# Optimization experiments

Hardware: AMD Instinct MI355X
Metric: run time of the kernel (lower is better)

Reference implementation:

```python
import jax, jax.numpy as jnp
import numpy as np

GROUPS = 2
EPS = 1e-5


def channel_shuffle(x, groups=2):
    b, c, h, w = x.shape
    x = x.reshape(b, groups, c // groups, h, w)
    x = jnp.transpose(x, (0, 2, 1, 3, 4))
    return x.reshape(b, c, h, w)


def binarize_weight(w):
    # w: (O, I/g, k, k). scaling_factor = mean |w| over (in,kh,kw), detached.
    scale = jax.lax.stop_gradient(jnp.mean(jnp.abs(w), axis=(1, 2, 3), keepdims=True))
    bw = scale * jnp.sign(w)
    cl = jnp.clip(w, -1.0, 1.0)
    # STE: forward value = bw, gradient flows through clamp
    return jax.lax.stop_gradient(bw) - jax.lax.stop_gradient(cl) + cl


@jax.custom_vjp
def bin_act(x):
    return jnp.sign(x)


def _bin_act_fwd(x):
    return jnp.sign(x), x


def _bin_act_bwd(x, g):
    scale = jnp.where((x >= 1.0) | (x <= -1.0), 0.01, 1.0)
    return (g * scale,)


bin_act.defvjp(_bin_act_fwd, _bin_act_bwd)


def grouped_bin_conv(x, w, pad):
    return jax.lax.conv_general_dilated(
        x, binarize_weight(w), window_strides=(1, 1),
        padding=[(pad, pad), (pad, pad)],
        dimension_numbers=('NCHW', 'OIHW', 'NCHW'),
        feature_group_count=GROUPS)


def batchnorm(x, gamma, beta):
    # training-mode BN: biased batch statistics over (N,H,W)
    mu = jnp.mean(x, axis=(0, 2, 3), keepdims=True)
    var = jnp.mean((x - mu) ** 2, axis=(0, 2, 3), keepdims=True)
    xn = (x - mu) * jax.lax.rsqrt(var + EPS)
    return xn * gamma[None, :, None, None] + beta[None, :, None, None]


def add_bias(x, b):
    return x + b[None, :, None, None]


def prelu(x, a):
    return jnp.where(x >= 0, x, a[None, :, None, None] * x)


def setup_inputs() -> dict:
    key = jax.random.key(0)
    ks = jax.random.split(key, 4)
    C, half = 256, 128
    x = jax.random.normal(ks[0], (32, C, 56, 56), dtype=jnp.float32)
    # two BinaryConvs (64,128,3,3) stacked -> grouped (128,128,3,3)
    w3 = jax.random.uniform(ks[1], (half, C // GROUPS, 3, 3), dtype=jnp.float32) * 0.001
    w1 = jax.random.uniform(ks[2], (half, C // GROUPS, 1, 1), dtype=jnp.float32) * 0.001
    z = jnp.zeros((C,), jnp.float32)
    return {
        'x': x, 'w3': w3, 'w1': w1,
        'b1': z, 'g1': jnp.ones((half,), jnp.float32), 'be1': jnp.zeros((half,), jnp.float32),
        'b2_1': z, 'a2': jnp.full((C,), 0.25, jnp.float32), 'b2_2': z,
        'b3_1': z, 'g3': jnp.ones((half,), jnp.float32), 'be3': jnp.zeros((half,), jnp.float32),
        'b4_1': z, 'a4': jnp.full((C,), 0.25, jnp.float32), 'b4_2': z,
    }


def reference(x, w3, w1, b1, g1, be1, b2_1, a2, b2_2, b3_1, g3, be3, b4_1, a4, b4_2):
    half = w3.shape[0]  # out_channel // 2 = 128
    x = channel_shuffle(x, GROUPS)
    x1 = bin_act(add_bias(x, b1))
    x1 = batchnorm(grouped_bin_conv(x1, w3, pad=1), g1, be1)
    x1_res = x[:, half:]
    x1 = x1 + x[:, :half]
    x2 = jnp.concatenate([x1, x1_res], axis=1)
    x2 = add_bias(prelu(add_bias(x2, b2_1), a2), b2_2)
    x2 = add_bias(x2, b3_1)
    x3 = bin_act(x2)
    x3 = batchnorm(grouped_bin_conv(x3, w1, pad=0), g3, be3)
    x3_res = x2[:, half:]
    x3 = x3 + x2[:, :half]
    x4 = jnp.concatenate([x3, x3_res], axis=1)
    x5 = add_bias(prelu(add_bias(x4, b4_1), a4), b4_2)
    return x5
```

## Files before the change

kernel.cpp:

```cpp
#include <hip/hip_runtime.h>
#include <stdint.h>

typedef unsigned short ushort_t;
typedef unsigned int uint_t;
typedef _Float16 half_t;

typedef float  float4_t __attribute__((ext_vector_type(4)));
typedef float  float2_t __attribute__((ext_vector_type(2)));
typedef _Float16 half4_t __attribute__((ext_vector_type(4)));
typedef _Float16 half2_t __attribute__((ext_vector_type(2)));
typedef uint_t uint4_t  __attribute__((ext_vector_type(4)));
typedef uint_t uint2_t  __attribute__((ext_vector_type(2)));

#define B_N 32
#define C_N 256
#define HALF_N 128
#define H_N 56
#define W_N 56
#define HW_N 3136
#define NPIX (B_N * HW_N)
#define EPS_D 1e-5
#define W3S 40
#define PWS 16

__global__ void prep_kernel(const float* __restrict__ w3, const float* __restrict__ w1,
                            uint_t* __restrict__ wbits3, uint_t* __restrict__ wbits1,
                            uint_t* __restrict__ popcw3,
                            double* __restrict__ scale3, double* __restrict__ scale1,
                            double* __restrict__ sums1, double* __restrict__ sums2,
                            uint_t* __restrict__ oflags) {
    __shared__ double red[128];
    __shared__ int ipw[2][9];
    __shared__ int flsh[2];
    int t = threadIdx.x;
    int blk = blockIdx.x;
    int lane = t & 63;
    int wv = t >> 6;
    if (blk == 0) {
        sums1[t] = 0.0; sums1[128 + t] = 0.0;
        sums2[t] = 0.0; sums2[128 + t] = 0.0;
    }
    if (blk < 128) {
        int o = blk;
        double acc = 0.0;
        int anynp = 0;
        #pragma unroll
        for (int j = 0; j < 9; ++j) {
            float v = w3[o * 1152 + t * 9 + j];
            acc += fabs((double)v);
            anynp |= (v <= 0.f) ? 1 : 0;
            unsigned long long b = __ballot(v > 0.f);
            if (lane == 0) {
                wbits3[o * W3S + j * 4 + wv * 2 + 0] = (uint_t)b;
                wbits3[o * W3S + j * 4 + wv * 2 + 1] = (uint_t)(b >> 32);
                ipw[wv][j] = __popcll(b);
            }
        }
        unsigned long long m = __ballot(anynp != 0);
        if (lane == 0) flsh[wv] = (m != 0ull) ? 1 : 0;
        red[t] = acc; __syncthreads();
        for (int s = 64; s > 0; s >>= 1) { if (t < s) red[t] += red[t + s]; __syncthreads(); }
        if (t == 0) { scale3[o] = red[0] / 1152.0; oflags[o] = (uint_t)(flsh[0] | flsh[1]); }
        if (t < 9) popcw3[o * PWS + t] = (uint_t)(ipw[0][t] + ipw[1][t]);
    } else {
        int o = blk - 128;
        float v = w1[o * 128 + t];
        unsigned long long b = __ballot(v > 0.f);
        unsigned long long m = __ballot(v <= 0.f);
        if (lane == 0) {
            wbits1[o * 8 + wv * 2 + 0] = (uint_t)b;
            wbits1[o * 8 + wv * 2 + 1] = (uint_t)(b >> 32);
            flsh[wv] = (m != 0ull) ? 1 : 0;
        }
        red[t] = fabs((double)v); __syncthreads();
        for (int s = 64; s > 0; s >>= 1) { if (t < s) red[t] += red[t + s]; __syncthreads(); }
        if (t == 0) { scale1[o] = red[0] / 128.0; oflags[128 + o] = (uint_t)(flsh[0] | flsh[1]); }
    }
}

__global__ __launch_bounds__(256) void sign1_kernel(const float* __restrict__ x,
                                                    const float* __restrict__ b1,
                                                    uint_t* __restrict__ vb,
                                                    const uint_t* __restrict__ oflags,
                                                    uint_t* __restrict__ fin) {
    __shared__ int fl[4];
    int t = threadIdx.x;
    if (blockIdx.x == 0 && blockIdx.y == 0) {
        int lane = t & 63, wv4 = t >> 6;
        uint_t f = oflags[t];
        unsigned long long m = __ballot(f != 0u);
        if (lane == 0) fl[wv4] = (m != 0ull) ? 1 : 0;
        __syncthreads();
        if (t == 0) { fin[0] = (uint_t)(fl[0] | fl[1]); fin[1] = (uint_t)(fl[2] | fl[3]); }
    }
    int p = blockIdx.x * 512 + t * 2;
    int cb = blockIdx.y * 32;
    int b = p / HW_N;
    int hw = p - b * HW_N;
    const float* xb = x + (size_t)b * C_N * HW_N + hw;
    uint_t w0 = 0, w1 = 0;
    #pragma unroll
    for (int j = 0; j < 32; ++j) {
        int c = cb + j;
        int src = ((c & 1) << 7) + (c >> 1);
        float2_t xv = *(const float2_t*)(xb + (size_t)src * HW_N);
        double bc = (double)b1[c];
        if ((double)xv[0] + bc > 0.0) w0 |= (1u << j);
        if ((double)xv[1] + bc > 0.0) w1 |= (1u << j);
    }
    uint2_t o2; o2[0] = w0; o2[1] = w1;
    *(uint2_t*)(vb + (size_t)(cb >> 5) * NPIX + p) = o2;
}

__global__ __launch_bounds__(256) void conv3_kernel(const uint_t* __restrict__ vb,
                                                    const uint_t* __restrict__ wbits3,
                                                    const uint_t* __restrict__ popcw3,
                                                    half_t* __restrict__ yh,
                                                    double* __restrict__ sums,
                                                    const uint_t* __restrict__ fin) {
    __shared__ short dlds[32][258];
    __shared__ int partS[8][32];
    __shared__ int partS2[8][32];
    int t = threadIdx.x;
    int lane = t & 63;
    int wv = t >> 6;
    bool fast = (fin[0] == 0u);
    int yb = blockIdx.y;
    if (fast && (yb & 1)) return;
    int g = yb >> 1;
    int oh = yb & 1;
    int o0 = g * 64 + oh * 32;
    int p = blockIdx.x * 256 + t;
    int hw = p % HW_N;
    int h = hw / W_N;
    int w = hw - h * W_N;
    const uint_t* vbase = vb + (size_t)g * 4 * NPIX;

    uint_t v[9][4];
    int inv[9];
    int nvalid = 0;
    #pragma unroll
    for (int j = 0; j < 9; ++j) {
        int kh = j / 3 - 1, kw = j - (j / 3) * 3 - 1;
        int hh = h + kh, ww = w + kw;
        bool valid = (hh >= 0) && (hh < H_N) && (ww >= 0) && (ww < W_N);
        inv[j] = valid ? 0 : 1;
        nvalid += valid ? 1 : 0;
        int off = p + kh * W_N + kw;
        #pragma unroll
        for (int q = 0; q < 4; ++q)
            v[j][q] = valid ? vbase[(size_t)q * NPIX + off] : 0u;
    }
    int base = 128 * nvalid;

    if (fast) {
        int P = 0;
        #pragma unroll
        for (int j = 0; j < 9; ++j)
            #pragma unroll
            for (int q = 0; q < 4; ++q)
                P += __popc(v[j][q]);
        int dot = 2 * P - base;
        yh[(size_t)o0 * NPIX + p] = (half_t)(float)dot;
        int s = dot, s2 = dot * dot;
        #pragma unroll
        for (int off = 32; off > 0; off >>= 1) {
            s  += __shfl_xor(s, off);
            s2 += __shfl_xor(s2, off);
        }
        if (lane == 0) { partS[0][wv] = s; partS2[0][wv] = s2; }
        __syncthreads();
        if (t == 0) {
            partS[1][0]  = partS[0][0] + partS[0][1] + partS[0][2] + partS[0][3];
            partS2[1][0] = partS2[0][0] + partS2[0][1] + partS2[0][2] + partS2[0][3];
        }
        __syncthreads();
        if (t < 64) {
            atomicAdd(&sums[o0 + t], (double)partS[1][0]);
            atomicAdd(&sums[128 + o0 + t], (double)partS2[1][0]);
        }
        return;
    }

    half_t* yrow = yh + (size_t)o0 * NPIX + p;
    for (int oi = 0; oi < 32; ++oi) {
        const uint_t* wo = wbits3 + (size_t)(o0 + oi) * W3S;
        const uint_t* pw = popcw3 + (size_t)(o0 + oi) * PWS;
        int acc = 0;
        #pragma unroll
        for (int j = 0; j < 9; ++j)
            #pragma unroll
            for (int q = 0; q < 4; ++q)
                acc += __popc(v[j][q] ^ wo[j * 4 + q]);
        int corr = 0;
        #pragma unroll
        for (int j = 0; j < 9; ++j) corr += inv[j] * (int)pw[j];
        int dot = base - 2 * (acc - corr);
        yrow[(size_t)oi * NPIX] = (half_t)(float)dot;
        dlds[oi][t] = (short)dot;
    }
    __syncthreads();
    {
        int o = t & 31, seg = t >> 5;
        const int* r32 = (const int*)(&dlds[o][seg * 32]);
        int S = 0, S2 = 0;
        #pragma unroll
        for (int j = 0; j < 16; ++j) {
            int pr = r32[j];
            int d0 = (int)(short)(pr & 0xffff);
            int d1 = pr >> 16;
            S += d0 + d1; S2 += d0 * d0 + d1 * d1;
        }
        partS[seg][o] = S; partS2[seg][o] = S2;
    }
    __syncthreads();
    if (t < 32) {
        int S = 0, S2 = 0;
        #pragma unroll
        for (int s8 = 0; s8 < 8; ++s8) { S += partS[s8][t]; S2 += partS2[s8][t]; }
        int c = o0 + t;
        atomicAdd(&sums[c], (double)S);
        atomicAdd(&sums[128 + c], (double)S2);
    }
}

__device__ __forceinline__ void coef_entry(const double* __restrict__ sums,
                                           const double* __restrict__ scale,
                                           const float* __restrict__ gamma,
                                           const float* __restrict__ beta,
                                           int c, double* coefL) {
    double M = (double)NPIX;
    double mean = sums[c] / M;
    double var = sums[128 + c] / M - mean * mean;
    double s = scale[c];
    double r = 1.0 / sqrt(s * s * var + EPS_D);
    double g = (double)gamma[c];
    coefL[c] = s * r * g;
    coefL[128 + c] = (double)beta[c] - s * mean * r * g;
}

__device__ __forceinline__ void coef_entry_f(const double* __restrict__ sums,
                                             const double* __restrict__ scale,
                                             const float* __restrict__ gamma,
                                             const float* __restrict__ beta,
                                             int c, float* cf) {
    double M = (double)NPIX;
    double mean = sums[c] / M;
    double var = sums[128 + c] / M - mean * mean;
    double s = scale[c];
    double r = 1.0 / sqrt(s * s * var + EPS_D);
    double g = (double)gamma[c];
    cf[c] = (float)(s * r * g);
    cf[128 + c] = (float)((double)beta[c] - s * mean * r * g);
}

__device__ __forceinline__ double x2_val(double xs, double K, bool hasy,
                                         const double* coef1, int c,
                                         const float* __restrict__ b2_1, const float* __restrict__ a2,
                                         const float* __restrict__ b2_2, const float* __restrict__ b3_1) {
    int ci = c & 127;
    double t = hasy ? (coef1[ci] * K + coef1[128 + ci] + xs) : xs;
    t += (double)b2_1[c];
    double a = (double)a2[c];
    t = (t >= 0.0) ? t : a * t;
    t += (double)b2_2[c];
    t += (double)b3_1[c];
    return t;
}

__global__ __launch_bounds__(256, 4) void x2c1_fast_kernel(
        const float* __restrict__ x, const half_t* __restrict__ y1h,
        const double* __restrict__ sums1, const double* __restrict__ scale3,
        const float* __restrict__ g1, const float* __restrict__ be1,
        const float* __restrict__ b2_1, const float* __restrict__ a2,
        const float* __restrict__ b2_2, const float* __restrict__ b3_1,
        half_t* __restrict__ y3h, double* __restrict__ sums2,
        const float* __restrict__ b4_1, const float* __restrict__ a4,
        const float* __restrict__ b4_2, float* __restrict__ out,
        const uint_t* __restrict__ fin) {
    if ((fin[0] | fin[1]) != 0u) return;
    __shared__ float tile[64][128];
    __shared__ double coefL[256];
    __shared__ uint_t shW[128][5];
    __shared__ int red[4];
    int t = threadIdx.x;
    int lane = t & 63;
    int w = t >> 6;
    int g = blockIdx.y;
    if (g == 0 && t < 128) coef_entry(sums1, scale3, g1, be1, t, coefL);

    int p0 = blockIdx.x * 128;
    int sp = p0 + 2 * lane;
    int sb = sp / HW_N;
    int shw = sp - sb * HW_N;
    const float* sbase = x + (size_t)sb * C_N * HW_N + shw;
    int pl = t & 127;
    int h = t >> 7;
    int p = p0 + pl;
    int b = p / HW_N;
    int hw = p - b * HW_N;
    __syncthreads();

    uint_t wd0 = 0, wd1 = 0;
    #pragma unroll
    for (int cp = 0; cp < 2; ++cp) {
        #pragma unroll
        for (int s = 0; s < 16; ++s) {
            int cl = w + 4 * s;
            int c = g * 128 + cp * 64 + cl;
            int src = ((c & 1) << 7) + (c >> 1);
            float2_t v = *(const float2_t*)(sbase + (size_t)src * HW_N);
            *(float2_t*)(&tile[cl][2 * lane]) = v;
        }
        __syncthreads();
        double K = 0.0;
        if (g == 0) K = (double)(float)y1h[(size_t)(cp * 64) * NPIX + p];
        uint_t bits = 0u;
        #pragma unroll
        for (int j = 0; j < 32; ++j) {
            int cl = h * 32 + j;
            int c = g * 128 + cp * 64 + cl;
            double xs = (double)tile[cl][pl];
            double v = x2_val(xs, K, g == 0, coefL, c, b2_1, a2, b2_2, b3_1);
            bits |= (v > 0.0) ? (1u << j) : 0u;
            if (g == 1) {
                float b41c = b4_1[c], a4c = a4[c], b42c = b4_2[c];
                float f0 = (float)v + b41c;
                f0 = (f0 >= 0.f) ? f0 : a4c * f0;
                f0 += b42c;
                out[((size_t)b * C_N + c) * HW_N + hw] = f0;
            }
        }
        shW[pl][cp * 2 + h] = bits;
        if (cp == 0) wd0 = bits; else wd1 = bits;
        (void)wd0; (void)wd1;
        __syncthreads();
    }

    uint_t W0 = shW[pl][0], W1 = shW[pl][1], W2 = shW[pl][2], W3 = shW[pl][3];
    int P = __popc(W0) + __popc(W1) + __popc(W2) + __popc(W3);
    int dot = 2 * P - 128;
    int obase = g * 64;
    if (h == 0) y3h[(size_t)obase * NPIX + p] = (half_t)(float)dot;
    int s = dot, s2 = dot * dot;
    #pragma unroll
    for (int off = 32; off > 0; off >>= 1) {
        s  += __shfl_xor(s, off);
        s2 += __shfl_xor(s2, off);
    }
    if (h == 0 && lane == 0) { red[w] = s; red[2 + w] = s2; }
    __syncthreads();
    if (t < 64) {
        int S  = red[0] + red[1];
        int S2 = red[2] + red[3];
        atomicAdd(&sums2[obase + t], (double)S);
        atomicAdd(&sums2[128 + obase + t], (double)S2);
    }
}

__global__ __launch_bounds__(256) void x2c1_gen_kernel(
        const float* __restrict__ x, const half_t* __restrict__ y1h,
        const double* __restrict__ sums1, const double* __restrict__ scale3,
        const float* __restrict__ g1, const float* __restrict__ be1,
        const float* __restrict__ b2_1, const float* __restrict__ a2,
        const float* __restrict__ b2_2, const float* __restrict__ b3_1,
        const uint_t* __restrict__ wbits1,
        half_t* __restrict__ y3h, double* __restrict__ sums2,
        const float* __restrict__ b4_1, const float* __restrict__ a4,
        const float* __restrict__ b4_2, float* __restrict__ out,
        const uint_t* __restrict__ fin) {
    if ((fin[0] | fin[1]) == 0u) return;
    __shared__ double coefL[256];
    __shared__ uint_t shW[128][5];
    __shared__ short dst[64][130];
    __shared__ int partS[4][64];
    __shared__ int partS2[4][64];
    int t = threadIdx.x;
    int lane = t & 63;
    int wv = t >> 6;
    int pl = t & 127;
    int ch = t >> 7;
    int g = blockIdx.y;
    bool fast3 = (fin[0] == 0u);
    bool fast1 = (fin[1] == 0u);
    if (g == 0 && t < 128) coef_entry(sums1, scale3, g1, be1, t, coefL);
    __syncthreads();

    int p = blockIdx.x * 128 + pl;
    int b = p / HW_N;
    int hw = p - b * HW_N;
    const float* xb = x + (size_t)b * C_N * HW_N + hw;

    uint_t wA = 0, wB = 0;
    if (g == 0) {
        if (fast3) {
            double K = (double)(float)y1h[(size_t)(ch * 64) * NPIX + p];
            #pragma unroll
            for (int wq = 0; wq < 2; ++wq) {
                uint_t bits = 0u;
                #pragma unroll
                for (int j = 0; j < 32; ++j) {
                    int c = ch * 64 + wq * 32 + j;
                    int src = ((c & 1) << 7) + (c >> 1);
                    double xs = (double)xb[(size_t)src * HW_N];
                    double v = x2_val(xs, K, true, coefL, c, b2_1, a2, b2_2, b3_1);
                    bits |= (v > 0.0) ? (1u << j) : 0u;
                }
                if (wq == 0) wA = bits; else wB = bits;
            }
        } else {
            #pragma unroll
            for (int wq = 0; wq < 2; ++wq) {
                uint_t bits = 0u;
                #pragma unroll
                for (int j = 0; j < 32; ++j) {
                    int c = ch * 64 + wq * 32 + j;
                    int src = ((c & 1) << 7) + (c >> 1);
                    double xs = (double)xb[(size_t)src * HW_N];
                    double K = (double)(float)y1h[(size_t)c * NPIX + p];
                    double v = x2_val(xs, K, true, coefL, c, b2_1, a2, b2_2, b3_1);
                    bits |= (v > 0.0) ? (1u << j) : 0u;
                }
                if (wq == 0) wA = bits; else wB = bits;
            }
        }
    } else {
        #pragma unroll
        for (int wq = 0; wq < 2; ++wq) {
            uint_t bits = 0u;
            #pragma unroll
            for (int j = 0; j < 32; ++j) {
                int c = 128 + ch * 64 + wq * 32 + j;
                int src = ((c & 1) << 7) + (c >> 1);
                double xs = (double)xb[(size_t)src * HW_N];
                double v = x2_val(xs, 0.0, false, coefL, c, b2_1, a2, b2_2, b3_1);
                bits |= (v > 0.0) ? (1u << j) : 0u;
                float b41c = b4_1[c], a4c = a4[c], b42c = b4_2[c];
                float f0 = (float)v + b41c;
                f0 = (f0 >= 0.f) ? f0 : a4c * f0;
                f0 += b42c;
                out[((size_t)b * C_N + c) * HW_N + hw] = f0;
            }
            if (wq == 0) wA = bits; else wB = bits;
        }
    }

    shW[pl][2 * ch + 0] = wA;
    shW[pl][2 * ch + 1] = wB;
    __syncthreads();
    uint_t W0 = shW[pl][0], W1 = shW[pl][1], W2 = shW[pl][2], W3 = shW[pl][3];

    int obase = g * 64;
    if (fast1) {
        if (ch == 0) {
            int P = __popc(W0) + __popc(W1) + __popc(W2) + __popc(W3);
            int dot = 2 * P - 128;
            y3h[(size_t)obase * NPIX + p] = (half_t)(float)dot;
            int s = dot, s2 = dot * dot;
            #pragma unroll
            for (int off = 32; off > 0; off >>= 1) {
                s  += __shfl_xor(s, off);
                s2 += __shfl_xor(s2, off);
            }
            if (lane == 0) { partS[0][wv] = s; partS2[0][wv] = s2; }
        }
        __syncthreads();
        if (t == 0) {
            partS[1][0]  = partS[0][0] + partS[0][1];
            partS2[1][0] = partS2[0][0] + partS2[0][1];
        }
        __syncthreads();
        if (t < 64) {
            atomicAdd(&sums2[obase + t], (double)partS[1][0]);
            atomicAdd(&sums2[128 + obase + t], (double)partS2[1][0]);
        }
        return;
    }

    #pragma unroll
    for (int oi = 0; oi < 32; ++oi) {
        int o = obase + ch * 32 + oi;
        const uint_t* wo = wbits1 + (size_t)o * 8;
        int acc = __popc(W0 ^ wo[0]) + __popc(W1 ^ wo[1])
                + __popc(W2 ^ wo[2]) + __popc(W3 ^ wo[3]);
        int dot = 128 - 2 * acc;
        y3h[(size_t)o * NPIX + p] = (half_t)(float)dot;
        dst[ch * 32 + oi][pl] = (short)dot;
    }
    __syncthreads();
    {
        int o = t & 63, seg = t >> 6;
        const int* r32 = (const int*)(&dst[o][seg * 32]);
        int S = 0, S2 = 0;
        #pragma unroll
        for (int j = 0; j < 16; ++j) {
            int pr = r32[j];
            int e0 = (int)(short)(pr & 0xffff);
            int e1 = pr >> 16;
            S += e0 + e1; S2 += e0 * e0 + e1 * e1;
        }
        partS[seg][o] = S; partS2[seg][o] = S2;
    }
    __syncthreads();
    if (t < 64) {
        int S  = partS[0][t] + partS[1][t] + partS[2][t] + partS[3][t];
        int S2 = partS2[0][t] + partS2[1][t] + partS2[2][t] + partS2[3][t];
        int c = obase + t;
        atomicAdd(&sums2[c], (double)S);
        atomicAdd(&sums2[128 + c], (double)S2);
    }
}

__global__ __launch_bounds__(256) void out_kernel(
        const float* __restrict__ x, const half_t* __restrict__ y1h,
        const half_t* __restrict__ y3h,
        const double* __restrict__ sums1, const double* __restrict__ scale3,
        const float* __restrict__ g1, const float* __restrict__ be1,
        const double* __restrict__ sums2, const double* __restrict__ scale1,
        const float* __restrict__ g3, const float* __restrict__ be3,
        const float* __restrict__ b2_1, const float* __restrict__ a2,
        const float* __restrict__ b2_2, const float* __restrict__ b3_1,
        const float* __restrict__ b4_1, const float* __restrict__ a4,
        const float* __restrict__ b4_2, float* __restrict__ out,
        const uint_t* __restrict__ fin) {
    __shared__ float c1f[256];
    __shared__ float c3f[256];
    int t = threadIdx.x;
    if (t < 128) coef_entry_f(sums1, scale3, g1, be1, t, c1f);
    else coef_entry_f(sums2, scale1, g3, be3, t - 128, c3f);
    __syncthreads();
    int c = blockIdx.y;
    int src = ((c & 1) << 7) + (c >> 1);
    int y1slice = (fin[0] == 0u) ? ((c < 64) ? 0 : 64) : c;
    int y3slice = (fin[1] == 0u) ? ((c < 64) ? 0 : 64) : c;
    float b21 = b2_1[c], aa2v = a2[c], b23 = b2_2[c] + b3_1[c];
    float b41 = b4_1[c], aa4v = a4[c], b42 = b4_2[c];
    float c1 = c1f[c], c1b = c1f[128 + c];
    float c3 = c3f[c], c3b = c3f[128 + c];
    const half_t* y1p = y1h + (size_t)y1slice * NPIX;
    const half_t* y3p = y3h + (size_t)y3slice * NPIX;
    #pragma unroll
    for (int i = 0; i < 2; ++i) {
        int p = blockIdx.x * 2048 + i * 1024 + t * 4;
        int b = p / HW_N;
        int hw = p - b * HW_N;
        float4_t xs = *(const float4_t*)(x + ((size_t)b * C_N + src) * HW_N + hw);
        half4_t y1v = *(const half4_t*)(y1p + p);
        half4_t y3v = *(const half4_t*)(y3p + p);
        float4_t ov;
        #pragma unroll
        for (int k = 0; k < 4; ++k) {
            float v = fmaf(c1, (float)y1v[k], c1b) + xs[k];
            v += b21;
            v = (v >= 0.f) ? v : aa2v * v;
            v += b23;
            float t2 = v;
            v = fmaf(c3, (float)y3v[k], c3b) + t2;
            v += b41;
            v = (v >= 0.f) ? v : aa4v * v;
            v += b42;
            ov[k] = v;
        }
        *(float4_t*)(out + ((size_t)b * C_N + c) * HW_N + hw) = ov;
    }
}

extern "C" void kernel_launch(void* const* d_in, const int* in_sizes, int n_in,
                              void* d_out, int out_size, void* d_ws, size_t ws_size,
                              hipStream_t stream) {
    const float* x    = (const float*)d_in[0];
    const float* w3   = (const float*)d_in[1];
    const float* w1   = (const float*)d_in[2];
    const float* b1   = (const float*)d_in[3];
    const float* g1   = (const float*)d_in[4];
    const float* be1  = (const float*)d_in[5];
    const float* b2_1 = (const float*)d_in[6];
    const float* a2   = (const float*)d_in[7];
    const float* b2_2 = (const float*)d_in[8];
    const float* b3_1 = (const float*)d_in[9];
    const float* g3   = (const float*)d_in[10];
    const float* be3  = (const float*)d_in[11];
    const float* b4_1 = (const float*)d_in[12];
    const float* a4   = (const float*)d_in[13];
    const float* b4_2 = (const float*)d_in[14];

    char* ws = (char*)d_ws;
    half_t* y1h    = (half_t*)(ws + 0);
    half_t* y3h    = (half_t*)(ws + 25690112);
    uint_t* wbits3 = (uint_t*)(ws + 51380224);
    uint_t* wbits1 = (uint_t*)(ws + 51400704);
    uint_t* popcw3 = (uint_t*)(ws + 51404800);
    double* scale3 = (double*)(ws + 51412992);
    double* scale1 = (double*)(ws + 51414016);
    double* sums1  = (double*)(ws + 51415040);
    double* sums2  = (double*)(ws + 51417088);
    uint_t* oflags = (uint_t*)(ws + 51419136);
    uint_t* fin    = (uint_t*)(ws + 51420160);

    uint_t* vb1 = (uint_t*)((char*)d_out + 0);
    float*  outp = (float*)d_out;

    prep_kernel<<<256, 128, 0, stream>>>(w3, w1, wbits3, wbits1, popcw3,
                                         scale3, scale1, sums1, sums2, oflags);
    sign1_kernel<<<dim3(NPIX / 512, 8), 256, 0, stream>>>(x, b1, vb1, oflags, fin);
    conv3_kernel<<<dim3(NPIX / 256, 4), 256, 0, stream>>>(vb1, wbits3, popcw3, y1h, sums1, fin);
    x2c1_fast_kernel<<<dim3(NPIX / 128, 2), 256, 0, stream>>>(x, y1h, sums1, scale3, g1, be1,
                                                              b2_1, a2, b2_2, b3_1,
                                                              y3h, sums2,
                                                              b4_1, a4, b4_2, outp, fin);
    x2c1_gen_kernel<<<dim3(NPIX / 128, 2), 256, 0, stream>>>(x, y1h, sums1, scale3, g1, be1,
                                                             b2_1, a2, b2_2, b3_1,
                                                             wbits1, y3h, sums2,
                                                             b4_1, a4, b4_2, outp, fin);
    out_kernel<<<dim3(NPIX / 2048, 128), 256, 0, stream>>>(x, y1h, y3h,
                                                           sums1, scale3, g1, be1,
                                                           sums2, scale1, g3, be3,
                                                           b2_1, a2, b2_2, b3_1,
                                                           b4_1, a4, b4_2, outp, fin);
}
```

Measured before the change: 316.4 us.

## Split fused x2/conv1 fast kernel into per-group kernels without LDS transpose tile

Replaces the single two-group fast kernel with two separate kernels, one per channel group. Each handles 64 pixels per block with four channel quarters, reading x directly instead of staging it through a shared-memory tile. This drops the 32KB LDS tile, the branch on group inside the hot loop and the cross-wave reduction, and lifts the forced occupancy hint. The cost is an extra launch, narrower per-thread global reads, and twice as many sums2 atomics, since each block covers 64 pixels instead of 128.

Measured after the change: 336.7 us. +6.4%, slower.

```diff
diff --git a/kernel.cpp b/kernel.cpp
--- a/kernel.cpp
+++ b/kernel.cpp
@@ -268,10 +268,56 @@
     return t;
 }
 
-__global__ __launch_bounds__(256, 4) void x2c1_fast_kernel(
+__global__ __launch_bounds__(256) void x2g0_fast_kernel(
         const float* __restrict__ x, const half_t* __restrict__ y1h,
         const double* __restrict__ sums1, const double* __restrict__ scale3,
         const float* __restrict__ g1, const float* __restrict__ be1,
+        const float* __restrict__ b2_1, const float* __restrict__ a2,
+        const float* __restrict__ b2_2, const float* __restrict__ b3_1,
+        half_t* __restrict__ y3h, double* __restrict__ sums2,
+        const uint_t* __restrict__ fin) {
+    if ((fin[0] | fin[1]) != 0u) return;
+    __shared__ double coefL[256];
+    __shared__ uint_t shW[64][5];
+    int t = threadIdx.x;
+    if (t < 128) coef_entry(sums1, scale3, g1, be1, t, coefL);
+    __syncthreads();
+    int ql = t & 63;
+    int qc = t >> 6;
+    int p = blockIdx.x * 64 + ql;
+    int b = p / HW_N;
+    int hw = p - b * HW_N;
+    const float* xb = x + (size_t)b * C_N * HW_N + hw;
+    double K = (double)(float)y1h[(size_t)((qc >> 1) * 64) * NPIX + p];
+    uint_t bits = 0u;
+    #pragma unroll
+    for (int j = 0; j < 32; ++j) {
+        int c = qc * 32 + j;
+        int src = ((c & 1) << 7) + (c >> 1);
+        double xs = (double)xb[(size_t)src * HW_N];
+        double v = x2_val(xs, K, true, coefL, c, b2_1, a2, b2_2, b3_1);
+        bits |= (v > 0.0) ? (1u << j) : 0u;
+    }
+    shW[ql][qc] = bits;
+    __syncthreads();
+    if (t < 64) {
+        uint_t W0 = shW[t][0], W1 = shW[t][1], W2 = shW[t][2], W3 = shW[t][3];
+        int P = __popc(W0) + __popc(W1) + __popc(W2) + __popc(W3);
+        int dot = 2 * P - 128;
+        y3h[p] = (half_t)(float)dot;
+        int s = dot, s2 = dot * dot;
+        #pragma unroll
+        for (int off = 32; off > 0; off >>= 1) {
+            s  += __shfl_xor(s, off);
+            s2 += __shfl_xor(s2, off);
+        }
+        atomicAdd(&sums2[t], (double)s);
+        atomicAdd(&sums2[128 + t], (double)s2);
+    }
+}
+
+__global__ __launch_bounds__(256) void x2g1_fast_kernel(
+        const float* __restrict__ x,
         const float* __restrict__ b2_1, const float* __restrict__ a2,
         const float* __restrict__ b2_2, const float* __restrict__ b3_1,
         half_t* __restrict__ y3h, double* __restrict__ sums2,
@@ -279,82 +325,47 @@
         const float* __restrict__ b4_2, float* __restrict__ out,
         const uint_t* __restrict__ fin) {
     if ((fin[0] | fin[1]) != 0u) return;
-    __shared__ float tile[64][128];
-    __shared__ double coefL[256];
-    __shared__ uint_t shW[128][5];
-    __shared__ int red[4];
+    __shared__ uint_t shW[64][5];
     int t = threadIdx.x;
-    int lane = t & 63;
-    int w = t >> 6;
-    int g = blockIdx.y;
-    if (g == 0 && t < 128) coef_entry(sums1, scale3, g1, be1, t, coefL);
-
-    int p0 = blockIdx.x * 128;
-    int sp = p0 + 2 * lane;
-    int sb = sp / HW_N;
-    int shw = sp - sb * HW_N;
-    const float* sbase = x + (size_t)sb * C_N * HW_N + shw;
-    int pl = t & 127;
-    int h = t >> 7;
-    int p = p0 + pl;
+    int ql = t & 63;
+    int qc = t >> 6;
+    int p = blockIdx.x * 64 + ql;
     int b = p / HW_N;
     int hw = p - b * HW_N;
-    __syncthreads();
-
-    uint_t wd0 = 0, wd1 = 0;
+    const float* xb = x + (size_t)b * C_N * HW_N + hw;
+    uint_t bits = 0u;
     #pragma unroll
-    for (int cp = 0; cp < 2; ++cp) {
-        #pragma unroll
-        for (int s = 0; s < 16; ++s) {
-            int cl = w + 4 * s;
-            int c = g * 128 + cp * 64 + cl;
-            int src = ((c & 1) << 7) + (c >> 1);
-            float2_t v = *(const float2_t*)(sbase + (size_t)src * HW_N);
-            *(float2_t*)(&tile[cl][2 * lane]) = v;
-        }
-        __syncthreads();
-        double K = 0.0;
-        if (g == 0) K = (double)(float)y1h[(size_t)(cp * 64) * NPIX + p];
-        uint_t bits = 0u;
-        #pragma unroll
-        for (int j = 0; j < 32; ++j) {
-            int cl = h * 32 + j;
-            int c = g * 128 + cp * 64 + cl;
-            double xs = (double)tile[cl][pl];
-            double v = x2_val(xs, K, g == 0, coefL, c, b2_1, a2, b2_2, b3_1);
-            bits |= (v > 0.0) ? (1u << j) : 0u;
-            if (g == 1) {
-                float b41c = b4_1[c], a4c = a4[c], b42c = b4_2[c];
-                float f0 = (float)v + b41c;
-                f0 = (f0 >= 0.f) ? f0 : a4c * f0;
-                f0 += b42c;
-                out[((size_t)b * C_N + c) * HW_N + hw] = f0;
-            }
-        }
-        shW[pl][cp * 2 + h] = bits;
-        if (cp == 0) wd0 = bits; else wd1 = bits;
-        (void)wd0; (void)wd1;
-        __syncthreads();
-    }
-
-    uint_t W0 = shW[pl][0], W1 = shW[pl][1], W2 = shW[pl][2], W3 = shW[pl][3];
-    int P = __popc(W0) + __popc(W1) + __popc(W2) + __popc(W3);
-    int dot = 2 * P - 128;
-    int obase = g * 64;
-    if (h == 0) y3h[(size_t)obase * NPIX + p] = (half_t)(float)dot;
-    int s = dot, s2 = dot * dot;
-    #pragma unroll
-    for (int off = 32; off > 0; off >>= 1) {
-        s  += __shfl_xor(s, off);
-        s2 += __shfl_xor(s2, off);
-    }
-    if (h == 0 && lane == 0) { red[w] = s; red[2 + w] = s2; }
+    for (int j = 0; j < 32; ++j) {
+        int c = 128 + qc * 32 + j;
+        int src = ((c & 1) << 7) + (c >> 1);
+        double xs = (double)xb[(size_t)src * HW_N];
+        double tt = xs;
+        tt += (double)b2_1[c];
+        double aa = (double)a2[c];
+        tt = (tt >= 0.0) ? tt : aa * tt;
+        tt += (double)b2_2[c];
+        tt += (double)b3_1[c];
+        bits |= (tt > 0.0) ? (1u << j) : 0u;
+        float f0 = (float)tt + b4_1[c];
+        f0 = (f0 >= 0.f) ? f0 : a4[c] * f0;
+        f0 += b4_2[c];
+        out[((size_t)b * C_N + c) * HW_N + hw] = f0;
+    }
+    shW[ql][qc] = bits;
     __syncthreads();
     if (t < 64) {
-        int S  = red[0] + red[1];
-        int S2 = red[2] + red[3];
-        atomicAdd(&sums2[obase + t], (double)S);
-        atomicAdd(&sums2[128 + obase + t], (double)S2);
+        uint_t W0 = shW[t][0], W1 = shW[t][1], W2 = shW[t][2], W3 = shW[t][3];
+        int P = __popc(W0) + __popc(W1) + __popc(W2) + __popc(W3);
+        int dot = 2 * P - 128;
+        y3h[(size_t)64 * NPIX + p] = (half_t)(float)dot;
+        int s = dot, s2 = dot * dot;
+        #pragma unroll
+        for (int off = 32; off > 0; off >>= 1) {
+            s  += __shfl_xor(s, off);
+            s2 += __shfl_xor(s2, off);
+        }
+        atomicAdd(&sums2[64 + t], (double)s);
+        atomicAdd(&sums2[192 + t], (double)s2);
     }
 }
 
@@ -604,10 +615,12 @@
                                          scale3, scale1, sums1, sums2, oflags);
     sign1_kernel<<<dim3(NPIX / 512, 8), 256, 0, stream>>>(x, b1, vb1, oflags, fin);
     conv3_kernel<<<dim3(NPIX / 256, 4), 256, 0, stream>>>(vb1, wbits3, popcw3, y1h, sums1, fin);
-    x2c1_fast_kernel<<<dim3(NPIX / 128, 2), 256, 0, stream>>>(x, y1h, sums1, scale3, g1, be1,
-                                                              b2_1, a2, b2_2, b3_1,
-                                                              y3h, sums2,
-                                                              b4_1, a4, b4_2, outp, fin);
+    x2g0_fast_kernel<<<NPIX / 64, 256, 0, stream>>>(x, y1h, sums1, scale3, g1, be1,
+                                                    b2_1, a2, b2_2, b3_1,
+                                                    y3h, sums2, fin);
+    x2g1_fast_kernel<<<NPIX / 64, 256, 0, stream>>>(x, b2_1, a2, b2_2, b3_1,
+                                                    y3h, sums2,
+                                                    b4_1, a4, b4_2, outp, fin);
     x2c1_gen_kernel<<<dim3(NPIX / 128, 2), 256, 0, stream>>>(x, y1h, sums1, scale3, g1, be1,
                                                              b2_1, a2, b2_2, b3_1,
                                                              wbits1, y3h, sums2,
```
